# Kernel optimization log

Hardware: AMD Instinct MI355X
Metric: run time of the kernel (lower is better)

The kernel has to match this reference:

```python
import jax, jax.numpy as jnp
import numpy as np

B, T, C, H = 4, 2048, 1024, 16
D = C // H

def setup_inputs() -> dict:
    key = jax.random.key(0)
    ks = jax.random.split(key, 9)
    s = 0.02
    return {
        "x": jax.random.normal(ks[0], (B, T, C), dtype=jnp.float32),
        "Wq": jax.random.normal(ks[1], (C, C), dtype=jnp.float32) * s,
        "bq": jnp.zeros((C,), dtype=jnp.float32),
        "Wk": jax.random.normal(ks[2], (C, C), dtype=jnp.float32) * s,
        "bk": jnp.zeros((C,), dtype=jnp.float32),
        "Wv": jax.random.normal(ks[3], (C, C), dtype=jnp.float32) * s,
        "bv": jnp.zeros((C,), dtype=jnp.float32),
        "Wo": jax.random.normal(ks[4], (C, C), dtype=jnp.float32) * s,
        "bo": jnp.zeros((C,), dtype=jnp.float32),
    }

def reference(x, Wq, bq, Wk, bk, Wv, bv, Wo, bo):
    # torch nn.Linear: y = x @ W.T + b
    q = x @ Wq.T + bq  # (B,T,C)
    k = x @ Wk.T + bk
    v = x @ Wv.T + bv
    # (B,H,T,D)
    q = q.reshape(B, T, H, D).transpose(0, 2, 1, 3)
    k = k.reshape(B, T, H, D).transpose(0, 2, 1, 3)
    v = v.reshape(B, T, H, D).transpose(0, 2, 1, 3)
    scale = 1.0 / jnp.sqrt(jnp.asarray(D, dtype=q.dtype))
    att = jnp.einsum("bhqd,bhkd->bhqk", q, k) * scale  # (B,H,T,T)
    causal = jnp.tril(jnp.ones((T, T), dtype=bool))
    att = jnp.where(causal[None, None], att, jnp.asarray(-jnp.inf, dtype=att.dtype))
    att = jax.nn.softmax(att, axis=-1)
    y = jnp.einsum("bhqk,bhkd->bhqd", att, v)  # (B,H,T,D)
    y = y.transpose(0, 2, 1, 3).reshape(B, T, C)
    return y @ Wo.T + bo
```

## Files before the change

kernel.cpp:

```cpp
#include <hip/hip_runtime.h>
#include <hip/hip_bf16.h>
#include <stdint.h>

typedef unsigned short u16;
typedef __bf16 bf16x8 __attribute__((ext_vector_type(8)));
typedef float f32x4 __attribute__((ext_vector_type(4)));
typedef float f32x16 __attribute__((ext_vector_type(16)));

#define NB 4
#define NT 2048
#define NC 1024
#define NH 16
#define ND 64
#define NM 8192
#define KVB 64

__device__ __forceinline__ u16 f2bf(float f) {
  union { float f; uint32_t u; } v; v.f = f;
  return (u16)((v.u + 0x7FFFu + ((v.u >> 16) & 1u)) >> 16);
}

__device__ __forceinline__ uint32_t pk2(float a, float b) {
  union { __hip_bfloat162 h; uint32_t u; } c;
  c.h = __float22bfloat162_rn(float2{a, b});
  return c.u;
}

__device__ __forceinline__ float fexp2(float x) {
#if __has_builtin(__builtin_amdgcn_exp2f)
  return __builtin_amdgcn_exp2f(x);
#else
  return exp2f(x);
#endif
}

__device__ __forceinline__ void g2l16(const void* g, void* l) {
  __builtin_amdgcn_global_load_lds((__attribute__((address_space(1))) const void*)g,
                                   (__attribute__((address_space(3))) void*)l,
                                   16, 0, 0);
}

__global__ __launch_bounds__(256) void cvtAll(
    const float* __restrict__ x,
    const float* __restrict__ w0, const float* __restrict__ w1,
    const float* __restrict__ w2, const float* __restrict__ w3,
    u16* __restrict__ ox, u16* o0, u16* o1, u16* o2, u16* o3) {
  const int b = blockIdx.x;
  const float* in;
  u16* out;
  int i;
  if (b < 8192) {
    in = x; out = ox; i = b * 256 + threadIdx.x;
  } else {
    const int w = (b - 8192) >> 10;
    const int wb = (b - 8192) & 1023;
    in = (w == 0) ? w0 : (w == 1) ? w1 : (w == 2) ? w2 : w3;
    out = (w == 0) ? o0 : (w == 1) ? o1 : (w == 2) ? o2 : o3;
    i = wb * 256 + threadIdx.x;
  }
  float4 v = ((const float4*)in)[i];
  ushort4 o;
  o.x = f2bf(v.x); o.y = f2bf(v.y); o.z = f2bf(v.z); o.w = f2bf(v.w);
  ((ushort4*)out)[i] = o;
}

template <int EPI>
__global__ __launch_bounds__(256, 2) void gemmDB(
    const u16* __restrict__ A,
    const u16* __restrict__ W0, const u16* __restrict__ W1, const u16* __restrict__ W2,
    const float* __restrict__ b0, const float* __restrict__ b1, const float* __restrict__ b2,
    void* o0, void* o1, void* o2, int K) {
  const int z = blockIdx.z;
  const u16* Bw = (z == 0) ? W0 : ((z == 1) ? W1 : W2);
  const float* bias = (z == 0) ? b0 : ((z == 1) ? b1 : b2);
  void* outp = (z == 0) ? o0 : ((z == 1) ? o1 : o2);

  __shared__ __align__(16) char SB[2][32768];

  const int lb = (blockIdx.x & 7) * (gridDim.x >> 3) + (blockIdx.x >> 3);
  const int m0 = (lb / 8) << 7;
  const int n0 = (lb % 8) << 7;
  const int t = threadIdx.x;
  const int wid = t >> 6, lane = t & 63;
  const int wm = wid >> 1, wn = wid & 1;
  const int lo = lane & 15, hi = lane >> 4;

  const int rr = t >> 3;
  const int sc = ((t & 7) ^ (rr & 7)) << 3;
  const u16* Asrc = A + (size_t)(m0 + rr) * K + sc;
  const u16* Bsrc = Bw + (size_t)(n0 + rr) * K + sc;

  f32x4 acc[4][4] = {};

  const int NTILES = K >> 6;

  auto STAGE = [&](int buf, int kt) {
#pragma unroll
    for (int j = 0; j < 4; ++j)
      g2l16(Asrc + (size_t)(j * 32) * K + kt * 64, SB[buf] + t * 16 + j * 4096);
#pragma unroll
    for (int j = 0; j < 4; ++j)
      g2l16(Bsrc + (size_t)(j * 32) * K + kt * 64,
            SB[buf] + 16384 + t * 16 + j * 4096);
  };

  STAGE(0, 0);
  __syncthreads();

  for (int kt = 0; kt < NTILES; ++kt) {
    const int cur = kt & 1;
    if (kt + 1 < NTILES) STAGE(cur ^ 1, kt + 1);

    const char* Ab = SB[cur];
    const char* Bb = SB[cur] + 16384;
#pragma unroll
    for (int kh = 0; kh < 2; ++kh) {
      const int slot = (((kh << 2) | hi) ^ (lo & 7)) << 4;
      bf16x8 af[4], bfr[4];
#pragma unroll
      for (int f = 0; f < 4; ++f)
        af[f] = *(const bf16x8*)(Ab + (wm * 64 + f * 16 + lo) * 128 + slot);
#pragma unroll
      for (int g = 0; g < 4; ++g)
        bfr[g] = *(const bf16x8*)(Bb + (wn * 64 + g * 16 + lo) * 128 + slot);
      __builtin_amdgcn_s_setprio(1);
#pragma unroll
      for (int f = 0; f < 4; ++f)
#pragma unroll
        for (int g = 0; g < 4; ++g)
          acc[f][g] = __builtin_amdgcn_mfma_f32_16x16x32_bf16(af[f], bfr[g],
                                                              acc[f][g], 0, 0, 0);
      __builtin_amdgcn_s_setprio(0);
    }
    __syncthreads();
  }

  const float scl = (EPI == 0 && z == 0) ? 0.125f * 1.44269504089f : 1.0f;
#pragma unroll
  for (int f = 0; f < 4; ++f) {
#pragma unroll
    for (int g = 0; g < 4; ++g) {
#pragma unroll
      for (int r = 0; r < 4; ++r) {
        const int rg = m0 + wm * 64 + f * 16 + hi * 4 + r;
        const int cg = n0 + wn * 64 + g * 16 + lo;
        const float v = (acc[f][g][r] + bias[cg]) * scl;
        if (EPI == 0) {
          const int bb = rg >> 11, tt = rg & (NT - 1);
          const int hh = cg >> 6, dd = cg & (ND - 1);
          size_t idx;
          if (z == 2)
            idx = ((size_t)(bb * NH + hh) * ND + dd) * NT + tt;
          else
            idx = ((size_t)(bb * NH + hh) * NT + tt) * ND + dd;
          ((u16*)outp)[idx] = f2bf(v);
        } else {
          ((float*)outp)[(size_t)rg * NC + cg] = v;
        }
      }
    }
  }
}

__global__ __launch_bounds__(512, 4) void flash5(const u16* __restrict__ Q,
                                                 const u16* __restrict__ Kg,
                                                 const u16* __restrict__ Vtg,
                                                 u16* __restrict__ Y) {
  __shared__ __align__(16) char LDS[65536];

  const int n = blockIdx.x;
  const int xcd = n & 7, slot = n >> 3;
  const int bh = (xcd << 3) | (slot >> 3);
  const int pt = slot & 7;
  const int qtB = 15 - pt;
  const int bb = bh >> 4, hh = bh & (NH - 1);
  const int tid = threadIdx.x;
  const int lane = tid & 63;
  const int grp = tid >> 8;
  const int ws4 = (tid >> 6) & 3;
  const int ql = lane & 31, h5 = lane >> 5;
  const int swz = (ql & 7) << 4;

  const u16* Qb = Q + (size_t)bh * NT * ND;
  const u16* Kb = Kg + (size_t)bh * NT * ND;
  const u16* Vb = Vtg + (size_t)bh * ND * NT;

  const int ntA = 2 * pt + 2;
  const int kvb1 = 15 - 2 * pt;
  const int q0wB = (qtB << 7) + (ws4 << 5);

  int q0w = grp ? q0wB : (pt << 7) + (ws4 << 5);
  int qg = q0w + ql;

  bf16x8 qf[4];
#pragma unroll
  for (int s = 0; s < 4; ++s)
    qf[s] = *(const bf16x8*)(Qb + (size_t)qg * ND + s * 16 + h5 * 8);

  f32x16 O0 = 0.f, O1 = 0.f;
  float lr = 0.f;

  const int tl = tid & 255;
  char* myL = LDS + (grp << 15);

  auto kvof = [&](int it) {
    return grp ? (kvb1 + it) : (it < ntA ? it : it - ntA);
  };

  auto STAGE = [&](int buf, int kv) {
#pragma unroll
    for (int p = 0; p < 2; ++p) {
      const int c = tl + (p << 8);
      const int row = c >> 3;
      const int so = ((c & 7) << 4) ^ ((row & 7) << 4);
      g2l16((const char*)(Kb + (size_t)((kv << 6) + row) * ND) + so,
            myL + (buf << 14) + c * 16);
      g2l16((const char*)(Vb + (size_t)row * NT + (kv << 6)) + so,
            myL + (buf << 14) + 8192 + c * 16);
    }
  };

  auto WRITEY = [&](const f32x16& A0, const f32x16& A1, float inv, int qgl) {
    u16* Yb = Y + ((size_t)bb * NT + qgl) * NC + hh * ND;
#pragma unroll
    for (int rq = 0; rq < 16; rq += 4) {
      const int dbase = 2 * rq + 4 * h5;
      uint2 w2;
      w2.x = pk2(A0[rq] * inv, A0[rq + 1] * inv);
      w2.y = pk2(A0[rq + 2] * inv, A0[rq + 3] * inv);
      *(uint2*)(Yb + dbase) = w2;
      w2.x = pk2(A1[rq] * inv, A1[rq + 1] * inv);
      w2.y = pk2(A1[rq + 2] * inv, A1[rq + 3] * inv);
      *(uint2*)(Yb + 32 + dbase) = w2;
    }
  };

  STAGE(0, kvof(0));
  __syncthreads();

  for (int it = 0; it < 17; ++it) {
    const int buf = it & 1;
    if (it < 16) STAGE(buf ^ 1, kvof(it + 1));

    if (!grp && it == ntA) {
      const float lt = lr + __shfl_xor(lr, 32, 64);
      WRITEY(O0, O1, 1.f / lt, qg);
      O0 = 0.f; O1 = 0.f; lr = 0.f;
      q0w = q0wB; qg = q0w + ql;
#pragma unroll
      for (int s = 0; s < 4; ++s)
        qf[s] = *(const bf16x8*)(Qb + (size_t)qg * ND + s * 16 + h5 * 8);
    }

    const int kv0 = kvof(it) << 6;
    const char* Kc = myL + (buf << 14);
    const char* Vc = Kc + 8192;

    f32x16 Sa0 = 0.f, Sa1 = 0.f;
    __builtin_amdgcn_s_setprio(1);
#pragma unroll
    for (int s = 0; s < 4; ++s) {
      bf16x8 kf0 = *(const bf16x8*)(Kc + ql * 128 + ((s * 32 + h5 * 16) ^ swz));
      bf16x8 kf1 = *(const bf16x8*)(Kc + (32 + ql) * 128 + ((s * 32 + h5 * 16) ^ swz));
      Sa0 = __builtin_amdgcn_mfma_f32_32x32x16_bf16(kf0, qf[s], Sa0, 0, 0, 0);
      Sa1 = __builtin_amdgcn_mfma_f32_32x32x16_bf16(kf1, qf[s], Sa1, 0, 0, 0);
    }
    __builtin_amdgcn_s_setprio(0);

    if (kv0 + 63 > q0w) {
#pragma unroll
      for (int r = 0; r < 16; ++r) {
        const int kvb = kv0 + (r & 3) + 8 * (r >> 2) + 4 * h5;
        if (kvb > qg) Sa0[r] = -3e38f;
        if (kvb + 32 > qg) Sa1[r] = -3e38f;
      }
    }

    float t0 = 0.f, t1 = 0.f, t2 = 0.f, t3 = 0.f;
#pragma unroll
    for (int r = 0; r < 16; r += 4) {
      const float a0 = fexp2(Sa0[r]),     a1 = fexp2(Sa0[r + 1]);
      const float a2 = fexp2(Sa0[r + 2]), a3 = fexp2(Sa0[r + 3]);
      const float b0 = fexp2(Sa1[r]),     b1 = fexp2(Sa1[r + 1]);
      const float b2 = fexp2(Sa1[r + 2]), b3 = fexp2(Sa1[r + 3]);
      Sa0[r] = a0; Sa0[r + 1] = a1; Sa0[r + 2] = a2; Sa0[r + 3] = a3;
      Sa1[r] = b0; Sa1[r + 1] = b1; Sa1[r + 2] = b2; Sa1[r + 3] = b3;
      t0 += a0 + b0; t1 += a1 + b1; t2 += a2 + b2; t3 += a3 + b3;
    }
    lr += (t0 + t1) + (t2 + t3);

    __builtin_amdgcn_s_setprio(1);
#pragma unroll
    for (int ks = 0; ks < 4; ++ks) {
      const int k0 = ks & 1;
      const f32x16& Sk = (ks < 2) ? Sa0 : Sa1;
      const uint32_t a0 = pk2(Sk[8 * k0],     Sk[8 * k0 + 1]);
      const uint32_t a1 = pk2(Sk[8 * k0 + 2], Sk[8 * k0 + 3]);
      const uint32_t b0 = pk2(Sk[8 * k0 + 4], Sk[8 * k0 + 5]);
      const uint32_t b1 = pk2(Sk[8 * k0 + 6], Sk[8 * k0 + 7]);
      const uint32_t c0 = h5 ? b0 : a0, c1 = h5 ? b1 : a1;
      const uint32_t d0 = h5 ? a0 : b0, d1 = h5 ? a1 : b1;
      const uint32_t x0 = __shfl_xor(d0, 32, 64);
      const uint32_t x1 = __shfl_xor(d1, 32, 64);
      union { uint32_t u[4]; bf16x8 v; } pf;
      pf.u[0] = h5 ? x0 : c0;
      pf.u[1] = h5 ? x1 : c1;
      pf.u[2] = h5 ? c0 : x0;
      pf.u[3] = h5 ? c1 : x1;
      bf16x8 vf0 = *(const bf16x8*)(Vc + ql * 128 + ((ks * 32 + h5 * 16) ^ swz));
      bf16x8 vf1 = *(const bf16x8*)(Vc + (32 + ql) * 128 + ((ks * 32 + h5 * 16) ^ swz));
      O0 = __builtin_amdgcn_mfma_f32_32x32x16_bf16(vf0, pf.v, O0, 0, 0, 0);
      O1 = __builtin_amdgcn_mfma_f32_32x32x16_bf16(vf1, pf.v, O1, 0, 0, 0);
    }
    __builtin_amdgcn_s_setprio(0);

    __syncthreads();
  }

  const int cslot = (ws4 << 6) + lane;
  char* cb = LDS + cslot * 136;
  if (!grp) {
#pragma unroll
    for (int j = 0; j < 8; ++j) {
      *(float2*)(cb + j * 8)      = float2{O0[2 * j], O0[2 * j + 1]};
      *(float2*)(cb + 64 + j * 8) = float2{O1[2 * j], O1[2 * j + 1]};
    }
    *(float*)(cb + 128) = lr;
  }
  __syncthreads();
  if (grp) {
#pragma unroll
    for (int j = 0; j < 8; ++j) {
      const float2 u = *(const float2*)(cb + j * 8);
      const float2 v = *(const float2*)(cb + 64 + j * 8);
      O0[2 * j] += u.x; O0[2 * j + 1] += u.y;
      O1[2 * j] += v.x; O1[2 * j + 1] += v.y;
    }
    lr += *(const float*)(cb + 128);
    const float lt = lr + __shfl_xor(lr, 32, 64);
    WRITEY(O0, O1, 1.f / lt, qg);
  }
}

extern "C" void kernel_launch(void* const* d_in, const int* in_sizes, int n_in,
                              void* d_out, int out_size, void* d_ws, size_t ws_size,
                              hipStream_t stream) {
  const float* x  = (const float*)d_in[0];
  const float* Wq = (const float*)d_in[1];
  const float* bq = (const float*)d_in[2];
  const float* Wk = (const float*)d_in[3];
  const float* bk = (const float*)d_in[4];
  const float* Wv = (const float*)d_in[5];
  const float* bv = (const float*)d_in[6];
  const float* Wo = (const float*)d_in[7];
  const float* bo = (const float*)d_in[8];

  const size_t SZ_X = (size_t)NM * NC * 2;
  const size_t SZ_W = (size_t)NC * NC * 2;
  char* ws = (char*)d_ws;
  u16* xb  = (u16*)ws;
  u16* wqb = (u16*)(ws + SZ_X);
  u16* wkb = (u16*)(ws + SZ_X + 1 * SZ_W);
  u16* wvb = (u16*)(ws + SZ_X + 2 * SZ_W);
  u16* wob = (u16*)(ws + SZ_X + 3 * SZ_W);
  u16* vb  = (u16*)(ws + SZ_X + 4 * SZ_W);
  u16* yb  = (u16*)(ws + 2 * SZ_X + 4 * SZ_W);
  u16* qb = (u16*)d_out;
  u16* kb = (u16*)((char*)d_out + SZ_X);

  if (ws_size < 3 * SZ_X + 4 * SZ_W) return;

  cvtAll<<<dim3(12288), 256, 0, stream>>>(x, Wq, Wk, Wv, Wo,
                                          xb, wqb, wkb, wvb, wob);

  gemmDB<0><<<dim3(512, 1, 3), 256, 0, stream>>>(
      xb, wqb, wkb, wvb, bq, bk, bv, qb, kb, vb, NC);

  flash5<<<dim3(512), 512, 0, stream>>>(qb, kb, vb, yb);

  gemmDB<1><<<dim3(512, 1, 1), 256, 0, stream>>>(
      yb, wob, wob, wob, bo, bo, bo, d_out, d_out, d_out, NC);
}
```

Measured before the change: 156.1 us.

## Use 256x256-tile 8-wave QKV projection GEMM with phased staging pipeline

Replaces the QKV projection GEMM (128x128 tiles, 256 threads, 3-D grid) with a new kernel that uses 256x256 tiles, 512 threads and 128 KB of double-buffered LDS. The new kernel interleaves global-to-LDS staging of the next k-tile with MFMA phases, using explicit vmcnt waits and barriers. The grid is 384 blocks, XCD-swizzled, with the Q/K/V selector folded into the block index. The aim is more data reuse per loaded tile and better overlap of memory and compute. The cost is large LDS use that limits occupancy, plus many barriers per k-tile. The output GEMM is simplified into a dedicated fp32 epilogue kernel.

```diff
diff --git a/kernel.cpp b/kernel.cpp
--- a/kernel.cpp
+++ b/kernel.cpp
@@ -64,17 +64,122 @@
   ((ushort4*)out)[i] = o;
 }
 
-template <int EPI>
-__global__ __launch_bounds__(256, 2) void gemmDB(
+__global__ __launch_bounds__(512, 2) void gemmKH(
     const u16* __restrict__ A,
     const u16* __restrict__ W0, const u16* __restrict__ W1, const u16* __restrict__ W2,
     const float* __restrict__ b0, const float* __restrict__ b1, const float* __restrict__ b2,
-    void* o0, void* o1, void* o2, int K) {
-  const int z = blockIdx.z;
+    u16* __restrict__ oq, u16* __restrict__ ok, u16* __restrict__ ov) {
+  constexpr int K = NC;
+  __shared__ __align__(16) char SB[2 * 65536];
+
+  const int lb = (blockIdx.x & 7) * 48 + (blockIdx.x >> 3);
+  const int z = lb >> 7;
+  const int tile = lb & 127;
   const u16* Bw = (z == 0) ? W0 : ((z == 1) ? W1 : W2);
   const float* bias = (z == 0) ? b0 : ((z == 1) ? b1 : b2);
-  void* outp = (z == 0) ? o0 : ((z == 1) ? o1 : o2);
-
+  u16* outp = (z == 0) ? oq : ((z == 1) ? ok : ov);
+
+  const int m0 = (tile >> 2) << 8;
+  const int n0 = (tile & 3) << 8;
+  const int t = threadIdx.x;
+  const int wid = t >> 6, lane = t & 63;
+  const int wm = wid >> 2, wn = wid & 3;
+  const int lo = lane & 15, hi = lane >> 4;
+  const int ch = (hi ^ ((lo >> 1) & 3)) << 4;
+
+  const int rr = t >> 2;
+  const int cs = (((t & 3) ^ ((t >> 3) & 3)) << 3);
+  const u16* Asrc = A + (size_t)(m0 + rr) * K + cs;
+  const u16* Bsrc = Bw + (size_t)(n0 + rr) * K + cs;
+
+  f32x4 acc[8][4] = {};
+
+  auto STAGEU = [&](int b, int kt, int u) {
+    const u16* s = ((u & 1) ? Bsrc : Asrc) + kt * 64 + (u >> 1) * 32;
+    char* d = SB + b * 65536 + ((u & 1) ? 32768 : 0) + (u >> 1) * 16384 + t * 16;
+    g2l16(s, d);
+    g2l16(s + (size_t)128 * K, d + 8192);
+  };
+
+  STAGEU(0, 0, 0); STAGEU(0, 0, 1); STAGEU(0, 0, 2); STAGEU(0, 0, 3);
+
+  bf16x8 bfr[4];
+
+  for (int kt = 0; kt < 16; ++kt) {
+    const int cb = (kt & 1) << 16;
+    const int nb = (kt & 1) ^ 1;
+    const bool st = (kt + 1 < 16);
+
+    asm volatile("s_waitcnt vmcnt(4)" ::: "memory");
+    __builtin_amdgcn_sched_barrier(0);
+    asm volatile("s_barrier" ::: "memory");
+    __builtin_amdgcn_sched_barrier(0);
+
+#pragma unroll
+    for (int ph = 0; ph < 4; ++ph) {
+      const int kh = ph >> 1, fh = ph & 1;
+      const char* Abase = SB + cb + kh * 16384;
+      const char* Bbase = SB + cb + 32768 + kh * 16384;
+      bf16x8 af[4];
+#pragma unroll
+      for (int f4 = 0; f4 < 4; ++f4)
+        af[f4] = *(const bf16x8*)(Abase + (wm * 128 + (fh * 4 + f4) * 16 + lo) * 64 + ch);
+      if (fh == 0) {
+#pragma unroll
+        for (int g = 0; g < 4; ++g)
+          bfr[g] = *(const bf16x8*)(Bbase + (wn * 64 + g * 16 + lo) * 64 + ch);
+      }
+      if (st) STAGEU(nb, kt + 1, ph);
+      __builtin_amdgcn_sched_barrier(0);
+      asm volatile("s_barrier" ::: "memory");
+      __builtin_amdgcn_sched_barrier(0);
+      __builtin_amdgcn_s_setprio(1);
+#pragma unroll
+      for (int f4 = 0; f4 < 4; ++f4)
+#pragma unroll
+        for (int g = 0; g < 4; ++g)
+          acc[fh * 4 + f4][g] = __builtin_amdgcn_mfma_f32_16x16x32_bf16(
+              af[f4], bfr[g], acc[fh * 4 + f4][g], 0, 0, 0);
+      __builtin_amdgcn_s_setprio(0);
+      __builtin_amdgcn_sched_barrier(0);
+      asm volatile("s_barrier" ::: "memory");
+      __builtin_amdgcn_sched_barrier(0);
+      if (ph == 1) {
+        if (st) asm volatile("s_waitcnt vmcnt(4)" ::: "memory");
+        else    asm volatile("s_waitcnt vmcnt(0)" ::: "memory");
+        __builtin_amdgcn_sched_barrier(0);
+        asm volatile("s_barrier" ::: "memory");
+        __builtin_amdgcn_sched_barrier(0);
+      }
+    }
+  }
+
+  const float scl = (z == 0) ? 0.125f * 1.44269504089f : 1.0f;
+#pragma unroll
+  for (int f = 0; f < 8; ++f) {
+#pragma unroll
+    for (int g = 0; g < 4; ++g) {
+#pragma unroll
+      for (int r = 0; r < 4; ++r) {
+        const int rg = m0 + wm * 128 + f * 16 + hi * 4 + r;
+        const int cg = n0 + wn * 64 + g * 16 + lo;
+        const float v = (acc[f][g][r] + bias[cg]) * scl;
+        const int bb = rg >> 11, tt = rg & (NT - 1);
+        const int hh = cg >> 6, dd = cg & (ND - 1);
+        size_t idx;
+        if (z == 2)
+          idx = ((size_t)(bb * NH + hh) * ND + dd) * NT + tt;
+        else
+          idx = ((size_t)(bb * NH + hh) * NT + tt) * ND + dd;
+        outp[idx] = f2bf(v);
+      }
+    }
+  }
+}
+
+__global__ __launch_bounds__(256, 2) void gemmDB(
+    const u16* __restrict__ A, const u16* __restrict__ W0,
+    const float* __restrict__ b0, float* __restrict__ outp, int K) {
   __shared__ __align__(16) char SB[2][32768];
 
   const int lb = (blockIdx.x & 7) * (gridDim.x >> 3) + (blockIdx.x >> 3);
@@ -88,10 +193,9 @@
   const int rr = t >> 3;
   const int sc = ((t & 7) ^ (rr & 7)) << 3;
   const u16* Asrc = A + (size_t)(m0 + rr) * K + sc;
-  const u16* Bsrc = Bw + (size_t)(n0 + rr) * K + sc;
+  const u16* Bsrc = W0 + (size_t)(n0 + rr) * K + sc;
 
   f32x4 acc[4][4] = {};
-
   const int NTILES = K >> 6;
 
   auto STAGE = [&](int buf, int kt) {
@@ -135,31 +239,16 @@
     __syncthreads();
   }
 
-  const float scl = (EPI == 0 && z == 0) ? 0.125f * 1.44269504089f : 1.0f;
-#pragma unroll
-  for (int f = 0; f < 4; ++f) {
-#pragma unroll
-    for (int g = 0; g < 4; ++g) {
+#pragma unroll
+  for (int f = 0; f < 4; ++f)
+#pragma unroll
+    for (int g = 0; g < 4; ++g)
 #pragma unroll
       for (int r = 0; r < 4; ++r) {
         const int rg = m0 + wm * 64 + f * 16 + hi * 4 + r;
         const int cg = n0 + wn * 64 + g * 16 + lo;
-        const float v = (acc[f][g][r] + bias[cg]) * scl;
-        if (EPI == 0) {
-          const int bb = rg >> 11, tt = rg & (NT - 1);
-          const int hh = cg >> 6, dd = cg & (ND - 1);
-          size_t idx;
-          if (z == 2)
-            idx = ((size_t)(bb * NH + hh) * ND + dd) * NT + tt;
-          else
-            idx = ((size_t)(bb * NH + hh) * NT + tt) * ND + dd;
-          ((u16*)outp)[idx] = f2bf(v);
-        } else {
-          ((float*)outp)[(size_t)rg * NC + cg] = v;
-        }
+        outp[(size_t)rg * NC + cg] = acc[f][g][r] + b0[cg];
       }
-    }
-  }
 }
 
 __global__ __launch_bounds__(512, 4) void flash5(const u16* __restrict__ Q,
@@ -373,11 +462,10 @@
   cvtAll<<<dim3(12288), 256, 0, stream>>>(x, Wq, Wk, Wv, Wo,
                                           xb, wqb, wkb, wvb, wob);
 
-  gemmDB<0><<<dim3(512, 1, 3), 256, 0, stream>>>(
-      xb, wqb, wkb, wvb, bq, bk, bv, qb, kb, vb, NC);
+  gemmKH<<<dim3(384), 512, 0, stream>>>(
+      xb, wqb, wkb, wvb, bq, bk, bv, qb, kb, vb);
 
   flash5<<<dim3(512), 512, 0, stream>>>(qb, kb, vb, yb);
 
-  gemmDB<1><<<dim3(512, 1, 1), 256, 0, stream>>>(
-      yb, wob, wob, wob, bo, bo, bo, d_out, d_out, d_out, NC);
-}
+  gemmDB<<<dim3(512), 256, 0, stream>>>(yb, wob, bo, (float*)d_out, NC);
+}
```

After: 200.6 us. 28.4% more time.
